# Performance work log

Measured on AMD Instinct MI355X. Metric: run time of the kernel, lower is better.

The kernel has to match this reference:

```python
import jax, jax.numpy as jnp
import numpy as np

N, D = 131072, 512
G, NG = 512, 256  # G groups of equal size NG, contiguous; N == G*NG
MARGIN, LAMBDA_CD, LAMBDA_CDD, LAMBDA_PCC, K_MARGIN = 2.0, 0.0, 1.0, 1.0, 0.02
EPS = 1e-6


def setup_inputs() -> dict:
    key = jax.random.key(0)
    k1, k2, k3, k4 = jax.random.split(key, 4)
    z_r = jax.random.normal(k1, (N, D), jnp.float32)
    z_r = z_r / jnp.linalg.norm(z_r, axis=-1, keepdims=True)
    z_v = jax.random.normal(k2, (N, D), jnp.float32)
    z_v = z_v / jnp.linalg.norm(z_v, axis=-1, keepdims=True)
    labels = jax.random.randint(k3, (N,), 0, 2)
    groups = jnp.repeat(jnp.arange(G), NG)  # contiguous equal-size groups
    var_lens = jax.random.randint(k4, (N,), 0, 10000)
    return {"z_r": z_r, "z_v": z_v, "labels": labels, "groups": groups, "var_lens": var_lens}


def reference(z_r, z_v, labels, groups, var_lens):
    # cosine distance per pair: [N]
    d = 1.0 - jnp.sum(z_r * z_v, axis=-1)

    mb = (labels == 0).astype(d.dtype)
    mp = (labels == 1).astype(d.dtype)
    nb, npos = mb.sum(), mp.sum()
    db_mean = jnp.sum(d * mb) / jnp.maximum(nb, 1.0)
    dp_mean = jnp.sum(d * mp) / jnp.maximum(npos, 1.0)

    l_cd = jnp.where(nb > 0, db_mean, 0.0)
    l_cdd = jnp.where((nb > 0) & (npos > 0),
                      jax.nn.relu(MARGIN + db_mean - dp_mean), 0.0)

    # --- per-group losses, vectorized over G equal-size contiguous groups ---
    d_g = d.reshape(G, NG)                                   # [G, n_g]
    v_g = var_lens.reshape(G, NG).astype(d.dtype)            # [G, n_g]

    # Pearson-style z-score matching loss (torch std is unbiased, ddof=1)
    v_std = jnp.std(v_g, axis=1, ddof=1)
    d_std = jnp.std(d_g, axis=1, ddof=1)
    v_z = (v_g - v_g.mean(axis=1, keepdims=True)) / (v_std + EPS)[:, None]
    d_z = (d_g - d_g.mean(axis=1, keepdims=True)) / (d_std + EPS)[:, None]
    corr_loss = jnp.mean((v_z - d_z) ** 2, axis=1)
    corr_loss = jnp.where((v_std > 0) & (d_std > 0), corr_loss, 0.0)

    # sort each group by var_len
    order = jnp.argsort(v_g, axis=1)
    v_s = jnp.take_along_axis(v_g, order, axis=1)            # [G, n_g]
    d_s = jnp.take_along_axis(d_g, order, axis=1)            # [G, n_g]

    # neighbor monotonicity violation
    neigh_viol = jnp.mean(jax.nn.relu(d_s[:, :-1] - d_s[:, 1:] + K_MARGIN), axis=1)

    # pairwise rank loss: dv[g,i,j] = v_s[g,j] - v_s[g,i] (matches torch unsqueeze(0)-unsqueeze(1))
    dv = v_s[:, None, :] - v_s[:, :, None]                   # [G, n_g, n_g]
    dd = d_s[:, None, :] - d_s[:, :, None]                   # [G, n_g, n_g]
    mask = (dv > 0).astype(d.dtype)
    cnt = mask.sum(axis=(1, 2))
    pair_sum = jnp.sum(jax.nn.relu(K_MARGIN - dd) * mask, axis=(1, 2))
    rank_loss = jnp.where(cnt > 0, pair_sum / jnp.maximum(cnt, 1.0), 0.0)

    group_loss = corr_loss + neigh_viol + rank_loss          # [G]
    # size-weighted sum; all groups have equal size NG -> plain mean
    l_pcc = jnp.mean(group_loss)

    total = LAMBDA_CD * l_cd + LAMBDA_CDD * l_cdd + LAMBDA_PCC * l_pcc
    return total, l_cdd, l_pcc, d
```

## Files before the change

### kernel.cpp

```cpp
#include <hip/hip_runtime.h>

#define NTOT   131072
#define GCNT   512
#define NGRP   256
#define KMARG  0.02f
#define CMARG  2.0f
#define EPSC   1e-6f

typedef float f4 __attribute__((ext_vector_type(4)));

template <int NW, int M>
__device__ __forceinline__ void block_sum_m(float* v, float* red) {
  const int t = threadIdx.x;
#pragma unroll
  for (int m = 0; m < M; ++m) {
#pragma unroll
    for (int off = 32; off; off >>= 1) v[m] += __shfl_down(v[m], off, 64);
  }
  __syncthreads();
  if ((t & 63) == 0) {
#pragma unroll
    for (int m = 0; m < M; ++m) red[(t >> 6) * M + m] = v[m];
  }
  __syncthreads();
#pragma unroll
  for (int m = 0; m < M; ++m) {
    float s = 0.0f;
#pragma unroll
    for (int i = 0; i < NW; ++i) s += red[i * M + m];
    v[m] = s;
  }
}

__device__ __forceinline__ float wave_sum(float v) {
#pragma unroll
  for (int off = 32; off; off >>= 1) v += __shfl_down(v, off, 64);
  return v;
}

__global__ __launch_bounds__(256) void fused_kernel(const float* __restrict__ zr,
                                                    const float* __restrict__ zv,
                                                    const int* __restrict__ labels,
                                                    const int* __restrict__ varl,
                                                    float* __restrict__ dvec,
                                                    float* __restrict__ gout) {
  __shared__ float  red[4 * 4];
  __shared__ float  sd[NGRP];
  __shared__ float2 skv[NGRP];
  __shared__ float  sdat[NGRP];
  const int g = blockIdx.x, t = threadIdx.x;
  const int wave = t >> 6, lane = t & 63;

  const size_t rowbase = (size_t)g * NGRP;
#pragma unroll 2
  for (int it = 0; it < NGRP / 8; ++it) {
    const int rg = it * 8 + wave * 2;
    const size_t row0 = rowbase + rg;
    const f4* r = (const f4*)zr + (row0 << 7);
    const f4* v = (const f4*)zv + (row0 << 7);
    f4 a0 = __builtin_nontemporal_load(r + lane);
    f4 b0 = v[lane];
    f4 a1 = __builtin_nontemporal_load(r + lane + 64);
    f4 b1 = v[lane + 64];
    f4 a2 = __builtin_nontemporal_load(r + lane + 128);
    f4 b2 = v[lane + 128];
    f4 a3 = __builtin_nontemporal_load(r + lane + 192);
    f4 b3 = v[lane + 192];
    f4 p = a0 * b0 + a1 * b1;
    f4 q = a2 * b2 + a3 * b3;
    float s0 = wave_sum(p.x + p.y + p.z + p.w);
    float s1 = wave_sum(q.x + q.y + q.z + q.w);
    if (lane == 0) {
      const float d0 = 1.0f - s0, d1 = 1.0f - s1;
      sd[rg]     = d0;
      sd[rg + 1] = d1;
      dvec[row0]     = d0;
      dvec[row0 + 1] = d1;
    }
  }
  __syncthreads();

  const int idx = g * NGRP + t;
  const float dv  = sd[t];
  const float vv  = (float)varl[idx];
  const int   lab = labels[idx];

  skv[t] = make_float2(vv, dv);

  float sA[4] = {dv, vv, (lab == 0) ? dv : 0.0f, (lab == 0) ? 1.0f : 0.0f};
  block_sum_m<4, 4>(sA, red);
  const float sumd = sA[0], sumv = sA[1], sb = sA[2], cb = sA[3];
  const float md = sumd * (1.0f / NGRP), mv = sumv * (1.0f / NGRP);

  const float vdev = vv - mv, ddev = dv - md;
  float sB[3] = {vdev * vdev, ddev * ddev, vdev * ddev};
  block_sum_m<4, 3>(sB, red);
  const float svv = sB[0], sdd = sB[1], svd = sB[2];
  const float vstd = sqrtf(svv * (1.0f / (NGRP - 1)));
  const float dstd = sqrtf(sdd * (1.0f / (NGRP - 1)));
  const float iv = 1.0f / (vstd + EPSC), id = 1.0f / (dstd + EPSC);
  float corr = (svv * iv * iv + sdd * id * id - 2.0f * svd * iv * id) * (1.0f / NGRP);
  corr = (vstd > 0.0f && dstd > 0.0f) ? corr : 0.0f;

  int rank = 0;
  float pc = 0.0f, ps = 0.0f;
  const float pre = KMARG + dv;
  for (int j = 0; j < NGRP; ++j) {
    const float2 kv = skv[j];
    const float vj = kv.x, dj = kv.y;
    if (vj > vv) {
      pc += 1.0f;
      ps += fmaxf(pre - dj, 0.0f);
    }
    rank += (vj < vv || (vj == vv && j < t)) ? 1 : 0;
  }
  sdat[rank] = dv;
  __syncthreads();
  const float nv = (t < NGRP - 1) ? fmaxf(sdat[t] - sdat[t + 1] + KMARG, 0.0f) : 0.0f;

  float sC[3] = {ps, pc, nv};
  block_sum_m<4, 3>(sC, red);
  const float rank_loss = (sC[1] > 0.0f) ? sC[0] / fmaxf(sC[1], 1.0f) : 0.0f;
  const float neigh = sC[2] * (1.0f / (NGRP - 1));

  if (t == 0) {
    gout[g]            = corr + neigh + rank_loss;
    gout[GCNT + g]     = sb;
    gout[2 * GCNT + g] = cb;
    gout[3 * GCNT + g] = sumd;
  }
}

__global__ __launch_bounds__(512) void final_kernel(const float* __restrict__ gout,
                                                    float* __restrict__ out) {
  __shared__ float red[8 * 4];
  const int t = threadIdx.x;
  float s[4] = {gout[t], gout[GCNT + t], gout[2 * GCNT + t], gout[3 * GCNT + t]};
  block_sum_m<8, 4>(s, red);
  if (t == 0) {
    const float L = s[0], SB = s[1], CB = s[2], SumD = s[3];
    const float SP = SumD - SB;
    const float CP = (float)NTOT - CB;
    const float db = SB / fmaxf(CB, 1.0f);
    const float dp = SP / fmaxf(CP, 1.0f);
    const float l_cdd = (CB > 0.0f && CP > 0.0f) ? fmaxf(CMARG + db - dp, 0.0f) : 0.0f;
    const float l_pcc = L * (1.0f / GCNT);
    out[0] = l_cdd + l_pcc;
    out[1] = l_cdd;
    out[2] = l_pcc;
  }
}

extern "C" void kernel_launch(void* const* d_in, const int* in_sizes, int n_in,
                              void* d_out, int out_size, void* d_ws, size_t ws_size,
                              hipStream_t stream) {
  const float* zr     = (const float*)d_in[0];
  const float* zv     = (const float*)d_in[1];
  const int*   labels = (const int*)d_in[2];
  const int*   varl   = (const int*)d_in[4];
  float* out  = (float*)d_out;
  float* dvec = out + 3;
  float* gws  = (float*)d_ws;

  fused_kernel<<<GCNT, 256, 0, stream>>>(zr, zv, labels, varl, dvec, gws);
  final_kernel<<<1, 512, 0, stream>>>(gws, out);
}
```

Measured before the change: 112.7 us.

## Stream cosine-distance rows through double-buffered LDS via async global_load_lds

Replaces direct register loads of z_r/z_v rows with per-wave double-buffered staging through LDS using global_load_lds. Each wave handles 64 contiguous rows and prefetches the next row pair while it consumes the current one, with explicit vmcnt waits. The aim is to keep more bytes in flight in this bandwidth-bound dot-product phase. The cost is 64KB of shared memory per block, which may limit occupancy. The hand-written waitcnt and buffer-reuse ordering could also be fragile.

```diff
diff --git a/kernel.cpp b/kernel.cpp
--- a/kernel.cpp
+++ b/kernel.cpp
@@ -9,6 +9,12 @@
 
 typedef float f4 __attribute__((ext_vector_type(4)));
 
+__device__ __forceinline__ void gld16(const f4* gsrc, f4* ldst) {
+  __builtin_amdgcn_global_load_lds(
+      (const __attribute__((address_space(1))) void*)gsrc,
+      (__attribute__((address_space(3))) void*)ldst, 16, 0, 0);
+}
+
 template <int NW, int M>
 __device__ __forceinline__ void block_sum_m(float* v, float* red) {
   const int t = threadIdx.x;
@@ -44,40 +50,69 @@
                                                     const int* __restrict__ varl,
                                                     float* __restrict__ dvec,
                                                     float* __restrict__ gout) {
+  __shared__ f4     stg[2][4][4][128];
   __shared__ float  red[4 * 4];
   __shared__ float  sd[NGRP];
   __shared__ float2 skv[NGRP];
   __shared__ float  sdat[NGRP];
   const int g = blockIdx.x, t = threadIdx.x;
   const int wave = t >> 6, lane = t & 63;
-
   const size_t rowbase = (size_t)g * NGRP;
-#pragma unroll 2
-  for (int it = 0; it < NGRP / 8; ++it) {
-    const int rg = it * 8 + wave * 2;
-    const size_t row0 = rowbase + rg;
-    const f4* r = (const f4*)zr + (row0 << 7);
-    const f4* v = (const f4*)zv + (row0 << 7);
-    f4 a0 = __builtin_nontemporal_load(r + lane);
-    f4 b0 = v[lane];
-    f4 a1 = __builtin_nontemporal_load(r + lane + 64);
-    f4 b1 = v[lane + 64];
-    f4 a2 = __builtin_nontemporal_load(r + lane + 128);
-    f4 b2 = v[lane + 128];
-    f4 a3 = __builtin_nontemporal_load(r + lane + 192);
-    f4 b3 = v[lane + 192];
-    f4 p = a0 * b0 + a1 * b1;
-    f4 q = a2 * b2 + a3 * b3;
-    float s0 = wave_sum(p.x + p.y + p.z + p.w);
-    float s1 = wave_sum(q.x + q.y + q.z + q.w);
-    if (lane == 0) {
-      const float d0 = 1.0f - s0, d1 = 1.0f - s1;
-      sd[rg]     = d0;
-      sd[rg + 1] = d1;
-      dvec[row0]     = d0;
-      dvec[row0 + 1] = d1;
-    }
-  }
+  const size_t wrow0   = rowbase + (size_t)wave * 64;
+
+  const f4* zr4 = (const f4*)zr;
+  const f4* zv4 = (const f4*)zv;
+
+#define STAGE(k, ph) do {                                                  \
+    const size_t r0_ = wrow0 + 2 * (size_t)(k);                            \
+    const f4* pr_ = zr4 + (r0_ << 7) + lane;                               \
+    const f4* pv_ = zv4 + (r0_ << 7) + lane;                               \
+    gld16(pr_,       &stg[ph][wave][0][0]);                                \
+    gld16(pr_ + 64,  &stg[ph][wave][0][64]);                               \
+    gld16(pr_ + 128, &stg[ph][wave][1][0]);                                \
+    gld16(pr_ + 192, &stg[ph][wave][1][64]);                               \
+    gld16(pv_,       &stg[ph][wave][2][0]);                                \
+    gld16(pv_ + 64,  &stg[ph][wave][2][64]);                               \
+    gld16(pv_ + 128, &stg[ph][wave][3][0]);                                \
+    gld16(pv_ + 192, &stg[ph][wave][3][64]);                               \
+  } while (0)
+
+#define CONSUME(k, ph) do {                                                \
+    f4 a0_ = stg[ph][wave][0][lane];                                       \
+    f4 a1_ = stg[ph][wave][0][lane + 64];                                  \
+    f4 c0_ = stg[ph][wave][2][lane];                                       \
+    f4 c1_ = stg[ph][wave][2][lane + 64];                                  \
+    f4 b0_ = stg[ph][wave][1][lane];                                       \
+    f4 b1_ = stg[ph][wave][1][lane + 64];                                  \
+    f4 d0_ = stg[ph][wave][3][lane];                                       \
+    f4 d1_ = stg[ph][wave][3][lane + 64];                                  \
+    f4 p_ = a0_ * c0_ + a1_ * c1_;                                         \
+    f4 q_ = b0_ * d0_ + b1_ * d1_;                                         \
+    float s0_ = wave_sum((p_.x + p_.y) + (p_.z + p_.w));                   \
+    float s1_ = wave_sum((q_.x + q_.y) + (q_.z + q_.w));                   \
+    const int rg_ = wave * 64 + 2 * (k);                                   \
+    if (lane == 0) {                                                       \
+      const float e0_ = 1.0f - s0_, e1_ = 1.0f - s1_;                      \
+      sd[rg_]     = e0_;                                                   \
+      sd[rg_ + 1] = e1_;                                                   \
+      dvec[wrow0 + 2 * (k)]     = e0_;                                     \
+      dvec[wrow0 + 2 * (k) + 1] = e1_;                                     \
+    }                                                                      \
+  } while (0)
+
+  STAGE(0, 0);
+#pragma unroll 1
+  for (int k = 0; k < 31; ++k) {
+    STAGE(k + 1, (k + 1) & 1);
+    asm volatile("s_waitcnt vmcnt(8)" ::: "memory");
+    __builtin_amdgcn_sched_barrier(0);
+    CONSUME(k, k & 1);
+  }
+  asm volatile("s_waitcnt vmcnt(0)" ::: "memory");
+  __builtin_amdgcn_sched_barrier(0);
+  CONSUME(31, 1);
+#undef STAGE
+#undef CONSUME
   __syncthreads();
 
   const int idx = g * NGRP + t;
```

Measured after the change: 138.7 us. 23.1% more time.
